# Performance work log

Hardware: AMD Instinct MI355X
Metric: run time of the kernel (lower is better)

## Reference

```python
import jax, jax.numpy as jnp
import numpy as np

BLOCK = 32  # 2**basic_block

def _hadamard(n):
    H = np.array([[1.0]], dtype=np.float32)
    while H.shape[0] < n:
        H = np.block([[H, H], [H, -H]])
    return H


def setup_inputs() -> dict:
    key = jax.random.key(0)
    ks = jax.random.split(key, 9)
    B, T, I, Hd, O = 64, 512, 128, 1024, 128
    sgn = lambda k, shp: jnp.where(jax.random.normal(k, shp) >= 0, 1.0, -1.0).astype(jnp.float32)
    return {
        "x": jax.random.normal(ks[0], (B, T, I), dtype=jnp.float32),
        "W_in": jax.random.normal(ks[1], (I, Hd), dtype=jnp.float32) / np.sqrt(I),
        "s1": sgn(ks[2], (Hd,)),                      # Binadamard sign vector (layer 1)
        "b1": 0.01 * jax.random.normal(ks[3], (Hd,), dtype=jnp.float32),
        "s2": sgn(ks[4], (Hd,)),                      # Binadamard sign vector (layer 2, full)
        "b2": 0.01 * jax.random.normal(ks[5], (Hd,), dtype=jnp.float32),
        "Wbn": sgn(ks[6], (Hd, Hd)) / np.sqrt(Hd),    # BinaryNorm: sign(W)/sqrt(n), materialized
        "W_out": jax.random.normal(ks[7], (Hd, O), dtype=jnp.float32) / np.sqrt(Hd),
        "b_out": jax.random.normal(ks[8], (O,), dtype=jnp.float32),
    }


def reference(x, W_in, s1, b1, s2, b2, Wbn, W_out, b_out):
    B, T, _ = x.shape
    Hd = s1.shape[0]
    Hb = jnp.asarray(_hadamard(BLOCK) / np.sqrt(BLOCK), dtype=x.dtype)   # [32,32]
    Hf = jnp.asarray(_hadamard(Hd) / np.sqrt(Hd), dtype=x.dtype)         # [Hd,Hd]
    u = jnp.einsum('bti,ih->tbh', x, W_in)  # precompute input projections, time-major

    def step(carry, u_t):
        h1, h2 = carry
        # layer 1: block-diagonal sign*Hadamard recurrence + input
        h1 = s1 * (h1.reshape(B, -1, BLOCK) @ Hb).reshape(B, Hd) + b1 + u_t
        h1b = jax.nn.relu(h1)
        # layer 2: full sign*Hadamard recurrence + binary-norm projection of h1b
        h2 = s2 * (h2 @ Hf) + b2 + h1b @ Wbn
        return (h1, h2), None

    h0 = jnp.zeros((B, Hd), dtype=x.dtype)
    (_, h2), _ = jax.lax.scan(step, (h0, h0), u)
    h2b = jax.nn.relu(h2)
    return h2b @ W_out + b_out
```

## Files before the change

### kernel.cpp

```cpp
#include <hip/hip_runtime.h>

#define B_ 64
#define T_ 512
#define I_ 128
#define H_ 1024
#define O_ 128

typedef unsigned short u16;
typedef unsigned int u32;
typedef __attribute__((ext_vector_type(8))) short short8v;
typedef __attribute__((ext_vector_type(4))) float float4v;

typedef __attribute__((address_space(1))) const void gvoid_t;
typedef __attribute__((address_space(3))) void svoid_t;

__device__ __forceinline__ u16 f2bf(float f) {
  union { float f; u32 u; } v; v.f = f;
  u32 r = v.u + 0x7FFF + ((v.u >> 16) & 1);
  return (u16)(r >> 16);
}
__device__ __forceinline__ float bf2f(u16 b) {
  union { u32 u; float f; } v; v.u = ((u32)b) << 16;
  return v.f;
}
__device__ __forceinline__ float bits2f(u32 b) {
  union { u32 u; float f; } v; v.u = b;
  return v.f;
}

__device__ __forceinline__ float fwht32(float x, int lane) {
#pragma unroll
  for (int s = 1; s <= 16; s <<= 1) {
    const float y = __shfl_xor(x, s);
    x = (lane & s) ? (y - x) : (x + y);
  }
  return x;
}

__device__ __forceinline__ void fwht32_reg(float* x) {
#pragma unroll
  for (int s = 1; s < 32; s <<= 1)
#pragma unroll
    for (int i = 0; i < 32; ++i)
      if (!(i & s)) { const float a = x[i], b = x[i | s]; x[i] = a + b; x[i | s] = a - b; }
}

__global__ __launch_bounds__(256) void prep_all(const float* __restrict__ x, const float* __restrict__ Wbn,
                                                const float* __restrict__ W_in, u16* __restrict__ xT,
                                                u16* __restrict__ WbnT, u16* __restrict__ WinT) {
  const int blk = blockIdx.x;
  if (blk < 4096) {
    const int idx = blk * 256 + threadIdx.x;
    const int n = idx >> 10, k = idx & 1023;
    WbnT[idx] = f2bf(Wbn[(size_t)k * 1024 + n]);
  } else if (blk < 4608) {
    const int idx = (blk - 4096) * 256 + threadIdx.x;
    const int n = idx >> 7, k = idx & 127;
    WinT[idx] = f2bf(W_in[(size_t)k * 1024 + n]);
  } else {
    const int idx = (blk - 4608) * 256 + threadIdx.x;
    const int i = idx & (I_ - 1);
    const int r = idx >> 7;
    const int b = r & (B_ - 1);
    const int t = r >> 6;
    xT[idx] = f2bf(x[((size_t)b * T_ + t) * I_ + i]);
  }
}

template <int K, bool BIAS>
__global__ __launch_bounds__(256) void gemm_bf16(const u16* __restrict__ A, const u16* __restrict__ Bt,
                                                 u16* __restrict__ C, const float* __restrict__ bias) {
  __shared__ u16 As[128 * 64];
  __shared__ u16 Bs[128 * 64];
  const int tid = threadIdx.x;
  const int bid = blockIdx.y * 256 + blockIdx.x;
  const int swz = (bid & 7) * 256 + (bid >> 3);
  const int bm = swz & 255, bn = swz >> 8;
  const int lane = tid & 63, w = tid >> 6;
  const int wr = w >> 1, wc = w & 1;
  const int l16 = lane & 15, lq = lane >> 4;

  float4v acc[4][4];
#pragma unroll
  for (int mi = 0; mi < 4; ++mi)
#pragma unroll
    for (int ni = 0; ni < 4; ++ni)
#pragma unroll
      for (int j = 0; j < 4; ++j) acc[mi][ni][j] = 0.f;

  const int srow = w * 32 + (lane >> 3);
  const int scol = (((lane & 7) ^ (lane >> 3)) << 3);
  const u16* Ag = A + (size_t)(bm * 128 + srow) * K + scol;
  const u16* Bg = Bt + (size_t)(bn * 128 + srow) * K + scol;

  for (int k0 = 0; k0 < K; k0 += 64) {
    __syncthreads();
#pragma unroll
    for (int i = 0; i < 4; ++i) {
      __builtin_amdgcn_global_load_lds((gvoid_t*)(Ag + k0 + (size_t)i * 8 * K),
                                       (svoid_t*)&As[(w * 32 + i * 8) * 64], 16, 0, 0);
      __builtin_amdgcn_global_load_lds((gvoid_t*)(Bg + k0 + (size_t)i * 8 * K),
                                       (svoid_t*)&Bs[(w * 32 + i * 8) * 64], 16, 0, 0);
    }
    __syncthreads();
#pragma unroll
    for (int ks = 0; ks < 2; ++ks) {
      short8v a[4], bf[4];
#pragma unroll
      for (int mi = 0; mi < 4; ++mi) {
        const int row = wr * 64 + mi * 16 + l16;
        a[mi] = *(const short8v*)&As[row * 64 + (((ks * 4 + lq) ^ (row & 7)) << 3)];
      }
#pragma unroll
      for (int ni = 0; ni < 4; ++ni) {
        const int row = wc * 64 + ni * 16 + l16;
        bf[ni] = *(const short8v*)&Bs[row * 64 + (((ks * 4 + lq) ^ (row & 7)) << 3)];
      }
#pragma unroll
      for (int mi = 0; mi < 4; ++mi)
#pragma unroll
        for (int ni = 0; ni < 4; ++ni)
          acc[mi][ni] = __builtin_amdgcn_mfma_f32_16x16x32_bf16(a[mi], bf[ni], acc[mi][ni], 0, 0, 0);
    }
  }

#pragma unroll
  for (int mi = 0; mi < 4; ++mi)
#pragma unroll
    for (int ni = 0; ni < 4; ++ni) {
      const int row = bm * 128 + wr * 64 + mi * 16 + lq * 4;
      const int col = bn * 128 + wc * 64 + ni * 16 + l16;
      const float bv = BIAS ? bias[col] : 0.f;
#pragma unroll
      for (int j = 0; j < 4; ++j) C[(size_t)(row + j) * H_ + col] = f2bf(acc[mi][ni][j] + bv);
    }
}

__global__ __launch_bounds__(1024) void h1_Pinit(const float* __restrict__ s1, float* __restrict__ P) {
  const int hb = blockIdx.x;
  const int tid = threadIdx.x;
  const int j = tid >> 5, r = tid & 31;
  const int lane = tid & 63;
  const float sc = s1[hb * 32 + r] * 0.17677669529663687f;
  float x = (r == j) ? 1.f : 0.f;
  for (int it = 0; it < 16; ++it) x = sc * fwht32(x, lane);
  P[(size_t)hb * 1024 + r * 32 + j] = x;
}

__global__ __launch_bounds__(64) void h1_local(const u16* __restrict__ u, const float* __restrict__ s1,
                                               float* __restrict__ Ybuf) {
  const int g = blockIdx.x * 64 + threadIdx.x;
  const int hb = g & 31, b = (g >> 5) & 63, chunk = g >> 11;
  float x[32], sc[32];
#pragma unroll
  for (int i = 0; i < 32; i += 4) {
    const float4 s4 = *(const float4*)&s1[hb * 32 + i];
    sc[i] = s4.x * 0.17677669529663687f;
    sc[i + 1] = s4.y * 0.17677669529663687f;
    sc[i + 2] = s4.z * 0.17677669529663687f;
    sc[i + 3] = s4.w * 0.17677669529663687f;
  }
#pragma unroll
  for (int i = 0; i < 32; ++i) x[i] = 0.f;
  const u16* up = u + ((size_t)(chunk * 16) * B_ + b) * H_ + hb * 32;
#pragma unroll 2
  for (int k = 0; k < 16; ++k) {
    u32 wv[16];
#pragma unroll
    for (int j = 0; j < 4; ++j) {
      const uint4 t4 = *(const uint4*)(up + (size_t)k * (B_ * H_) + j * 8);
      wv[4 * j] = t4.x; wv[4 * j + 1] = t4.y; wv[4 * j + 2] = t4.z; wv[4 * j + 3] = t4.w;
    }
    fwht32_reg(x);
#pragma unroll
    for (int i2 = 0; i2 < 16; ++i2) {
      x[2 * i2]     = fmaf(sc[2 * i2],     x[2 * i2],     bits2f(wv[i2] << 16));
      x[2 * i2 + 1] = fmaf(sc[2 * i2 + 1], x[2 * i2 + 1], bits2f(wv[i2] & 0xFFFF0000u));
    }
  }
  float* yp = Ybuf + (size_t)g * 32;
#pragma unroll
  for (int i = 0; i < 32; i += 4) {
    float4 o; o.x = x[i]; o.y = x[i + 1]; o.z = x[i + 2]; o.w = x[i + 3];
    *(float4*)(yp + i) = o;
  }
}

__global__ __launch_bounds__(64) void h1_carry(const float* __restrict__ P, const float* __restrict__ Ybuf,
                                               float* __restrict__ Zbuf) {
  const int hpair = blockIdx.x, b = blockIdx.y;
  const int lane = threadIdx.x;
  const int r = lane & 31, hb = hpair * 2 + (lane >> 5);
  const float* Prow = P + (size_t)hb * 1024 + r * 32;
  float pr[32];
#pragma unroll
  for (int j = 0; j < 32; ++j) pr[j] = Prow[j];
  float z = 0.f;
  const int base = lane & 32;
  for (int c = 0; c < 32; ++c) {
    Zbuf[(((size_t)c * 64 + b) * 32 + hb) * 32 + r] = z;
    if (c < 31) {
      const float yv = Ybuf[(((size_t)c * 64 + b) * 32 + hb) * 32 + r];
      float zn = 0.f;
#pragma unroll
      for (int j = 0; j < 32; ++j) zn = fmaf(pr[j], __shfl(z, base + j), zn);
      z = zn + yv;
    }
  }
}

__global__ __launch_bounds__(64) void h1_apply(u16* __restrict__ u, const float* __restrict__ s1,
                                               const float* __restrict__ Zbuf) {
  const int g = blockIdx.x * 64 + threadIdx.x;
  const int hb = g & 31, b = (g >> 5) & 63, chunk = g >> 11;
  float x[32], sc[32];
#pragma unroll
  for (int i = 0; i < 32; i += 4) {
    const float4 s4 = *(const float4*)&s1[hb * 32 + i];
    sc[i] = s4.x * 0.17677669529663687f;
    sc[i + 1] = s4.y * 0.17677669529663687f;
    sc[i + 2] = s4.z * 0.17677669529663687f;
    sc[i + 3] = s4.w * 0.17677669529663687f;
  }
  const float* zp = Zbuf + (size_t)g * 32;
#pragma unroll
  for (int i = 0; i < 32; i += 4) {
    const float4 z4 = *(const float4*)(zp + i);
    x[i] = z4.x; x[i + 1] = z4.y; x[i + 2] = z4.z; x[i + 3] = z4.w;
  }
  u16* up = u + ((size_t)(chunk * 16) * B_ + b) * H_ + hb * 32;
#pragma unroll 2
  for (int k = 0; k < 16; ++k) {
    u32 wv[16];
#pragma unroll
    for (int j = 0; j < 4; ++j) {
      const uint4 t4 = *(const uint4*)(up + (size_t)k * (B_ * H_) + j * 8);
      wv[4 * j] = t4.x; wv[4 * j + 1] = t4.y; wv[4 * j + 2] = t4.z; wv[4 * j + 3] = t4.w;
    }
    fwht32_reg(x);
#pragma unroll
    for (int i2 = 0; i2 < 16; ++i2) {
      x[2 * i2]     = fmaf(sc[2 * i2],     x[2 * i2],     bits2f(wv[i2] << 16));
      x[2 * i2 + 1] = fmaf(sc[2 * i2 + 1], x[2 * i2 + 1], bits2f(wv[i2] & 0xFFFF0000u));
    }
    u32 ov[16];
#pragma unroll
    for (int i2 = 0; i2 < 16; ++i2) {
      const u32 lo = f2bf(fmaxf(x[2 * i2], 0.f));
      const u32 hi = f2bf(fmaxf(x[2 * i2 + 1], 0.f));
      ov[i2] = lo | (hi << 16);
    }
#pragma unroll
    for (int j = 0; j < 4; ++j) {
      uint4 t4; t4.x = ov[4 * j]; t4.y = ov[4 * j + 1]; t4.z = ov[4 * j + 2]; t4.w = ov[4 * j + 3];
      *(uint4*)(up + (size_t)k * (B_ * H_) + j * 8) = t4;
    }
  }
}

__device__ __forceinline__ void fwht1024(float* x, int lane) {
#pragma unroll
  for (int s = 1; s < 16; s <<= 1)
#pragma unroll
    for (int r = 0; r < 16; ++r)
      if (!(r & s)) { float a0 = x[r], b0 = x[r | s]; x[r] = a0 + b0; x[r | s] = a0 - b0; }
#pragma unroll
  for (int s = 0; s < 6; ++s) {
    const int m = 1 << s;
    const bool hi = (lane & m) != 0;
#pragma unroll
    for (int r = 0; r < 16; ++r) {
      const float y = __shfl_xor(x[r], m);
      x[r] = hi ? (y - x[r]) : (x[r] + y);
    }
  }
}

__global__ __launch_bounds__(256) void fwht_chunk(const u16* __restrict__ V, const float* __restrict__ s2,
                                                  u16* __restrict__ A32, u16* __restrict__ Y) {
  const int W = blockIdx.x * 4 + (threadIdx.x >> 6);
  const int lane = threadIdx.x & 63;
  float x[16], sc[16];
  if (W < 1024) {
#pragma unroll
    for (int r = 0; r < 16; ++r) {
      const int idx = r * 64 + lane;
      sc[r] = s2[idx] * 0.03125f;
      x[r] = (idx == W) ? 1.f : 0.f;
    }
    for (int it = 0; it < 32; ++it) {
#pragma unroll
      for (int r = 0; r < 16; ++r) x[r] *= sc[r];
      fwht1024(x, lane);
    }
    u16* dst = A32 + (size_t)W * H_ + lane;
#pragma unroll
    for (int r = 0; r < 16; ++r) dst[r * 64] = f2bf(x[r]);
  } else {
    const int W2 = W - 1024;
    const int c = W2 >> 6, b = W2 & 63;
#pragma unroll
    for (int r = 0; r < 16; ++r) { sc[r] = s2[r * 64 + lane] * 0.03125f; x[r] = 0.f; }
    const u16* p = V + ((size_t)(c * 32) * B_ + b) * H_ + lane;
    const size_t stride = (size_t)B_ * H_;
    u16 v[16];
#pragma unroll
    for (int r = 0; r < 16; ++r) v[r] = p[r * 64];
    for (int j = 0; j < 32; ++j) {
      u16 vn[16];
      if (j + 1 < 32) {
        const u16* pn = p + (size_t)(j + 1) * stride;
#pragma unroll
        for (int r = 0; r < 16; ++r) vn[r] = pn[r * 64];
      }
      fwht1024(x, lane);
#pragma unroll
      for (int r = 0; r < 16; ++r) x[r] = sc[r] * x[r] + bf2f(v[r]);
      if (j + 1 < 32) {
#pragma unroll
        for (int r = 0; r < 16; ++r) v[r] = vn[r];
      }
    }
    u16* dst = Y + ((size_t)c * B_ + b) * H_ + lane;
#pragma unroll
    for (int r = 0; r < 16; ++r) dst[r * 64] = f2bf(x[r]);
  }
}

template <bool FIRST, bool LAST>
__global__ __launch_bounds__(256) void combine(const u16* __restrict__ Zold, const u16* __restrict__ Yc,
                                               const u16* __restrict__ A32, u16* __restrict__ Znew,
                                               float* __restrict__ h2out) {
  const int rt = blockIdx.x >> 6, nt = blockIdx.x & 63;
  const int tid = threadIdx.x;
  __shared__ float red[4][16][16];
  if (!FIRST) {
    const int w = tid >> 6, lane = tid & 63, l16 = lane & 15, lq = lane >> 4;
    float4v acc = {0.f, 0.f, 0.f, 0.f};
    const u16* Ap = Zold + (size_t)(rt * 16 + l16) * H_ + w * 256 + lq * 8;
    const u16* Bp = A32 + (size_t)(nt * 16 + l16) * H_ + w * 256 + lq * 8;
#pragma unroll
    for (int ks = 0; ks < 8; ++ks) {
      short8v a = *(const short8v*)(Ap + ks * 32);
      short8v bb = *(const short8v*)(Bp + ks * 32);
      acc = __builtin_amdgcn_mfma_f32_16x16x32_bf16(a, bb, acc, 0, 0, 0);
    }
#pragma unroll
    for (int j = 0; j < 4; ++j) red[w][lq * 4 + j][l16] = acc[j];
    __syncthreads();
  } else {
    __syncthreads();
  }
  const int row = tid >> 4, col = tid & 15;
  float s = 0.f;
  if (!FIRST) s = red[0][row][col] + red[1][row][col] + red[2][row][col] + red[3][row][col];
  const int b = rt * 16 + row, n = nt * 16 + col;
  s += bf2f(Yc[(size_t)b * H_ + n]);
  if (LAST) h2out[(size_t)b * H_ + n] = s;
  else Znew[(size_t)b * H_ + n] = f2bf(s);
}

__global__ __launch_bounds__(128) void final_out(const float* __restrict__ h2, const float* __restrict__ W_out,
                                                 const float* __restrict__ b_out, float* __restrict__ out) {
  __shared__ float hrow[H_];
  const int b = blockIdx.x, o = threadIdx.x;
  for (int i = o; i < H_; i += 128) hrow[i] = fmaxf(h2[(size_t)b * H_ + i], 0.f);
  __syncthreads();
  float acc = b_out[o];
  for (int h = 0; h < H_; ++h) acc = fmaf(hrow[h], W_out[(size_t)h * O_ + o], acc);
  out[b * O_ + o] = acc;
}

extern "C" void kernel_launch(void* const* d_in, const int* in_sizes, int n_in,
                              void* d_out, int out_size, void* d_ws, size_t ws_size,
                              hipStream_t stream) {
  const float* x     = (const float*)d_in[0];
  const float* W_in  = (const float*)d_in[1];
  const float* s1    = (const float*)d_in[2];
  const float* b1    = (const float*)d_in[3];
  const float* s2    = (const float*)d_in[4];
  const float* b2    = (const float*)d_in[5];
  const float* Wbn   = (const float*)d_in[6];
  const float* W_out = (const float*)d_in[7];
  const float* b_out = (const float*)d_in[8];
  float* out = (float*)d_out;

  char* ws = (char*)d_ws;
  u16* u      = (u16*)ws;
  u16* V      = (u16*)(ws + 67108864);
  float* P1   = (float*)(ws + 67108864);
  float* Zbuf = (float*)(ws + 69206016);
  u16* xT     = (u16*)(ws + 134217728);
  float* Ybuf = (float*)(ws + 134217728);
  u16* WbnT   = (u16*)(ws + 142606336);
  u16* WinT   = (u16*)(ws + 144703488);
  u16* A32    = (u16*)(ws + 134217728);
  u16* Y      = (u16*)(ws + 136314880);
  u16* Zb0    = (u16*)(ws + 138412032);
  u16* Zb1    = (u16*)(ws + 138543104);
  float* h2   = (float*)(ws + 138674176);

  prep_all<<<20992, 256, 0, stream>>>(x, Wbn, W_in, xT, WbnT, WinT);
  h1_Pinit<<<32, 1024, 0, stream>>>(s1, P1);
  gemm_bf16<128, true><<<dim3(256, 8), 256, 0, stream>>>(xT, WinT, u, b1);
  h1_local<<<1024, 64, 0, stream>>>(u, s1, Ybuf);
  h1_carry<<<dim3(16, 64), 64, 0, stream>>>(P1, Ybuf, Zbuf);
  h1_apply<<<1024, 64, 0, stream>>>(u, s1, Zbuf);
  gemm_bf16<1024, true><<<dim3(256, 8), 256, 0, stream>>>(u, WbnT, V, b2);
  fwht_chunk<<<512, 256, 0, stream>>>(V, s2, A32, Y);

  u16* Zb[2] = {Zb0, Zb1};
  combine<true, false><<<256, 256, 0, stream>>>(nullptr, Y, A32, Zb[0], nullptr);
  for (int c = 1; c < 15; ++c)
    combine<false, false><<<256, 256, 0, stream>>>(Zb[(c + 1) & 1], Y + (size_t)c * B_ * H_, A32,
                                                   Zb[c & 1], nullptr);
  combine<false, true><<<256, 256, 0, stream>>>(Zb[0], Y + (size_t)15 * B_ * H_, A32, nullptr, h2);

  final_out<<<64, 128, 0, stream>>>(h2, W_out, b_out, out);
}
```

Measured before the change: 370.6 us.

## Compute 1024-point FWHT per half-wave via register transforms and LDS transpose

Replaces the wavefront-wide 1024-point Walsh-Hadamard transform, which used 16 values per lane and six rounds of cross-lane shuffles, with a 32x32 decomposition. Each 32-lane half-wave holds 32 values per lane, runs two in-register 32-point FWHTs, and swaps between them through a padded shared-memory transpose. The layout flips every step, so sign vectors and input loads alternate between contiguous vector loads and strided loads, and the grid is halved. The change also drops the block-index swizzle from the bf16 GEMM. It trades shuffle traffic for LDS traffic and much higher register pressure (about 96 floats for x plus two sign arrays), which may lower occupancy.

New measurement: 327.8 us. -11.5%, faster.

```diff
diff --git a/kernel.cpp b/kernel.cpp
--- a/kernel.cpp
+++ b/kernel.cpp
@@ -43,6 +43,13 @@
 #pragma unroll
     for (int i = 0; i < 32; ++i)
       if (!(i & s)) { const float a = x[i], b = x[i | s]; x[i] = a + b; x[i | s] = a - b; }
+}
+
+__device__ __forceinline__ void transpose32(float* x, float (*T)[33], int t) {
+#pragma unroll
+  for (int c = 0; c < 32; ++c) T[t][c] = x[c];
+#pragma unroll
+  for (int c = 0; c < 32; ++c) x[c] = T[c][t];
 }
 
 __global__ __launch_bounds__(256) void prep_all(const float* __restrict__ x, const float* __restrict__ Wbn,
@@ -73,9 +80,7 @@
   __shared__ u16 As[128 * 64];
   __shared__ u16 Bs[128 * 64];
   const int tid = threadIdx.x;
-  const int bid = blockIdx.y * 256 + blockIdx.x;
-  const int swz = (bid & 7) * 256 + (bid >> 3);
-  const int bm = swz & 255, bn = swz >> 8;
+  const int bm = blockIdx.x, bn = blockIdx.y;
   const int lane = tid & 63, w = tid >> 6;
   const int wr = w >> 1, wc = w & 1;
   const int l16 = lane & 15, lq = lane >> 4;
@@ -258,72 +263,91 @@
   }
 }
 
-__device__ __forceinline__ void fwht1024(float* x, int lane) {
-#pragma unroll
-  for (int s = 1; s < 16; s <<= 1)
-#pragma unroll
-    for (int r = 0; r < 16; ++r)
-      if (!(r & s)) { float a0 = x[r], b0 = x[r | s]; x[r] = a0 + b0; x[r | s] = a0 - b0; }
-#pragma unroll
-  for (int s = 0; s < 6; ++s) {
-    const int m = 1 << s;
-    const bool hi = (lane & m) != 0;
-#pragma unroll
-    for (int r = 0; r < 16; ++r) {
-      const float y = __shfl_xor(x[r], m);
-      x[r] = hi ? (y - x[r]) : (x[r] + y);
-    }
-  }
-}
-
 __global__ __launch_bounds__(256) void fwht_chunk(const u16* __restrict__ V, const float* __restrict__ s2,
                                                   u16* __restrict__ A32, u16* __restrict__ Y) {
-  const int W = blockIdx.x * 4 + (threadIdx.x >> 6);
+  __shared__ float tr[4][2][32][33];
+  const int wv = threadIdx.x >> 6;
   const int lane = threadIdx.x & 63;
-  float x[16], sc[16];
-  if (W < 1024) {
-#pragma unroll
-    for (int r = 0; r < 16; ++r) {
-      const int idx = r * 64 + lane;
-      sc[r] = s2[idx] * 0.03125f;
-      x[r] = (idx == W) ? 1.f : 0.f;
-    }
-    for (int it = 0; it < 32; ++it) {
-#pragma unroll
-      for (int r = 0; r < 16; ++r) x[r] *= sc[r];
-      fwht1024(x, lane);
-    }
-    u16* dst = A32 + (size_t)W * H_ + lane;
-#pragma unroll
-    for (int r = 0; r < 16; ++r) dst[r * 64] = f2bf(x[r]);
+  const int slot = lane >> 5, t = lane & 31;
+  float (*T)[33] = tr[wv][slot];
+  const int gs = blockIdx.x * 8 + wv * 2 + slot;
+
+  float x[32], s0[32], s1[32];
+#pragma unroll
+  for (int c = 0; c < 32; ++c) {
+    s0[c] = s2[t * 32 + c] * 0.03125f;
+    s1[c] = s2[c * 32 + t] * 0.03125f;
+  }
+
+  if (gs < 1024) {
+    const int W = gs;
+#pragma unroll
+    for (int c = 0; c < 32; ++c) x[c] = (t * 32 + c == W) ? 1.f : 0.f;
+    for (int j = 0; j < 32; ++j) {
+      if (j & 1) {
+#pragma unroll
+        for (int c = 0; c < 32; ++c) x[c] *= s1[c];
+      } else {
+#pragma unroll
+        for (int c = 0; c < 32; ++c) x[c] *= s0[c];
+      }
+      fwht32_reg(x);
+      transpose32(x, T, t);
+      fwht32_reg(x);
+    }
+    u16* dst = A32 + (size_t)W * H_ + t * 32;
+    u32 ov[16];
+#pragma unroll
+    for (int c = 0; c < 16; ++c) ov[c] = (u32)f2bf(x[2 * c]) | ((u32)f2bf(x[2 * c + 1]) << 16);
+#pragma unroll
+    for (int j = 0; j < 4; ++j) {
+      uint4 t4; t4.x = ov[4 * j]; t4.y = ov[4 * j + 1]; t4.z = ov[4 * j + 2]; t4.w = ov[4 * j + 3];
+      *(uint4*)(dst + j * 8) = t4;
+    }
   } else {
-    const int W2 = W - 1024;
-    const int c = W2 >> 6, b = W2 & 63;
-#pragma unroll
-    for (int r = 0; r < 16; ++r) { sc[r] = s2[r * 64 + lane] * 0.03125f; x[r] = 0.f; }
-    const u16* p = V + ((size_t)(c * 32) * B_ + b) * H_ + lane;
-    const size_t stride = (size_t)B_ * H_;
-    u16 v[16];
-#pragma unroll
-    for (int r = 0; r < 16; ++r) v[r] = p[r * 64];
+    const int s = gs - 1024;
+    const int c0 = s >> 6, b = s & 63;
+    const u16* Vbase = V + ((size_t)(c0 * 32) * B_ + b) * H_;
+#pragma unroll
+    for (int c = 0; c < 32; ++c) x[c] = 0.f;
     for (int j = 0; j < 32; ++j) {
-      u16 vn[16];
-      if (j + 1 < 32) {
-        const u16* pn = p + (size_t)(j + 1) * stride;
-#pragma unroll
-        for (int r = 0; r < 16; ++r) vn[r] = pn[r * 64];
+      const u16* vrow = Vbase + (size_t)j * (B_ * H_);
+      const int pe = (j + 1) & 1;
+      u32 vpk[16];
+      u16 vsc[32];
+      if (pe == 0) {
+#pragma unroll
+        for (int q = 0; q < 4; ++q) {
+          const uint4 t4 = *(const uint4*)(vrow + t * 32 + q * 8);
+          vpk[4 * q] = t4.x; vpk[4 * q + 1] = t4.y; vpk[4 * q + 2] = t4.z; vpk[4 * q + 3] = t4.w;
+        }
+      } else {
+#pragma unroll
+        for (int c = 0; c < 32; ++c) vsc[c] = vrow[c * 32 + t];
       }
-      fwht1024(x, lane);
-#pragma unroll
-      for (int r = 0; r < 16; ++r) x[r] = sc[r] * x[r] + bf2f(v[r]);
-      if (j + 1 < 32) {
-#pragma unroll
-        for (int r = 0; r < 16; ++r) v[r] = vn[r];
+      fwht32_reg(x);
+      transpose32(x, T, t);
+      fwht32_reg(x);
+      if (pe == 0) {
+#pragma unroll
+        for (int c = 0; c < 16; ++c) {
+          x[2 * c]     = fmaf(s0[2 * c],     x[2 * c],     bits2f(vpk[c] << 16));
+          x[2 * c + 1] = fmaf(s0[2 * c + 1], x[2 * c + 1], bits2f(vpk[c] & 0xFFFF0000u));
+        }
+      } else {
+#pragma unroll
+        for (int c = 0; c < 32; ++c) x[c] = fmaf(s1[c], x[c], bf2f(vsc[c]));
       }
     }
-    u16* dst = Y + ((size_t)c * B_ + b) * H_ + lane;
-#pragma unroll
-    for (int r = 0; r < 16; ++r) dst[r * 64] = f2bf(x[r]);
+    u16* dst = Y + ((size_t)c0 * B_ + b) * H_ + t * 32;
+    u32 ov[16];
+#pragma unroll
+    for (int c = 0; c < 16; ++c) ov[c] = (u32)f2bf(x[2 * c]) | ((u32)f2bf(x[2 * c + 1]) << 16);
+#pragma unroll
+    for (int j = 0; j < 4; ++j) {
+      uint4 t4; t4.x = ov[4 * j]; t4.y = ov[4 * j + 1]; t4.z = ov[4 * j + 2]; t4.w = ov[4 * j + 3];
+      *(uint4*)(dst + j * 8) = t4;
+    }
   }
 }
 
@@ -407,7 +431,7 @@
   h1_carry<<<dim3(16, 64), 64, 0, stream>>>(P1, Ybuf, Zbuf);
   h1_apply<<<1024, 64, 0, stream>>>(u, s1, Zbuf);
   gemm_bf16<1024, true><<<dim3(256, 8), 256, 0, stream>>>(u, WbnT, V, b2);
-  fwht_chunk<<<512, 256, 0, stream>>>(V, s2, A32, Y);
+  fwht_chunk<<<256, 256, 0, stream>>>(V, s2, A32, Y);
 
   u16* Zb[2] = {Zb0, Zb1};
   combine<true, false><<<256, 256, 0, stream>>>(nullptr, Y, A32, Zb[0], nullptr);
```
